# Performance work log

Measured on AMD Instinct MI355X. Metric: run time of the kernel, lower is better.

## Reference

```python
import jax, jax.numpy as jnp
import numpy as np

N_NODES = 50000
N_EDGES = 1_600_000
IN_CH = 128
OUT_CH = 64
HEADS = 2
NEG_SLOPE = 0.2  # PyG GATConv default negative_slope


def setup_inputs() -> dict:
    key = jax.random.key(0)
    ks = jax.random.split(key, 8)
    x = jax.random.normal(ks[0], (N_NODES, IN_CH), dtype=jnp.float32)
    edge_index = jax.random.randint(ks[1], (2, N_EDGES), 0, N_NODES, dtype=jnp.int64)
    edge_weight = jax.random.uniform(ks[2], (N_EDGES,), dtype=jnp.float32)
    W = jax.random.normal(ks[3], (IN_CH, HEADS * OUT_CH), dtype=jnp.float32) * (1.0 / np.sqrt(IN_CH))
    att_src = jax.random.normal(ks[4], (HEADS, OUT_CH), dtype=jnp.float32) * (1.0 / np.sqrt(OUT_CH))
    att_dst = jax.random.normal(ks[5], (HEADS, OUT_CH), dtype=jnp.float32) * (1.0 / np.sqrt(OUT_CH))
    bias = jnp.zeros((HEADS * OUT_CH,), dtype=jnp.float32)
    return {"x": x, "edge_index": edge_index, "edge_weight": edge_weight,
            "W": W, "att_src": att_src, "att_dst": att_dst, "bias": bias}


def reference(x, edge_index, edge_weight, W, att_src, att_dst, bias):
    # GATLayer: zero-masking is a no-op multiply (x * (x != 0)), kept for faithfulness.
    x_masked = x * (x != 0.0).astype(x.dtype)

    # GATConv (concat=True, add_self_loops=True). edge_weight is passed as edge_attr
    # but edge_dim is None, so it does not enter the attention math (legacy PyG behavior).
    n = x.shape[0]
    xp = (x_masked @ W).reshape(n, HEADS, OUT_CH)  # [N, H, C]

    # add self loops
    loops = jnp.arange(n, dtype=edge_index.dtype)
    src = jnp.concatenate([edge_index[0], loops])
    dst = jnp.concatenate([edge_index[1], loops])

    a_src = jnp.einsum('nhc,hc->nh', xp, att_src)  # [N, H]
    a_dst = jnp.einsum('nhc,hc->nh', xp, att_dst)  # [N, H]

    alpha = jax.nn.leaky_relu(a_src[src] + a_dst[dst], NEG_SLOPE)  # [E', H]

    # per-destination segment softmax
    m = jax.ops.segment_max(alpha, dst, num_segments=n)
    e = jnp.exp(alpha - m[dst])
    s = jax.ops.segment_sum(e, dst, num_segments=n)
    alpha = e / (s[dst] + 1e-16)

    # dropout on attention coefficients skipped (eval mode / deterministic baseline)
    msg = alpha[:, :, None] * xp[src]  # [E', H, C]
    out = jax.ops.segment_sum(msg, dst, num_segments=n)  # [N, H, C]
    return out.reshape(n, HEADS * OUT_CH) + bias
```

## Files before the change

### kernel.cpp

```cpp
#include <hip/hip_runtime.h>
#include <hip/hip_bf16.h>

#define NN 50000
#define NE 1600000
#define NE2 (NE + NN)
#define NEG_SLOPE 0.2f
#define NBUCK 196
#define BCAP 10240
#define P1E 4096
#define P1B ((NE2 + P1E - 1) / P1E)

__device__ __forceinline__ float bflo(unsigned u) { return __uint_as_float(u << 16); }
__device__ __forceinline__ float bfhi(unsigned u) { return __uint_as_float(u & 0xffff0000u); }
__device__ __forceinline__ float rlanef(float v, int l) {
    return __uint_as_float(__builtin_amdgcn_readlane(__float_as_uint(v), l));
}

__global__ __launch_bounds__(256, 4) void k_gemm(const float* __restrict__ x,
                                                 const float* __restrict__ W,
                                                 const float* __restrict__ att_src,
                                                 const float* __restrict__ att_dst,
                                                 __hip_bfloat16* __restrict__ xpb,
                                                 float* __restrict__ a4) {
    __shared__ float xl[64][128];
    const int tid = threadIdx.x;
    const int n0 = blockIdx.x * 64;
    const int rows_here = min(64, NN - n0);
    {
        const float4* xg = (const float4*)(x + (size_t)n0 * 128);
        float4* xl4 = (float4*)&xl[0][0];
        const int cnt = rows_here * 32;
        for (int i = tid; i < cnt; i += 256) xl4[i] = xg[i];
    }
    __syncthreads();

    const int c = tid & 127;
    const int half = tid >> 7;
    const int h = c >> 6;
    const int cc = c & 63;
    const float at_s = att_src[h * 64 + cc];
    const float at_d = att_dst[h * 64 + cc];

    float acc[32];
    #pragma unroll
    for (int r = 0; r < 32; r++) acc[r] = 0.f;

    #pragma unroll 2
    for (int kq = 0; kq < 32; kq++) {
        const float w0 = W[(kq * 4 + 0) * 128 + c];
        const float w1 = W[(kq * 4 + 1) * 128 + c];
        const float w2 = W[(kq * 4 + 2) * 128 + c];
        const float w3 = W[(kq * 4 + 3) * 128 + c];
        #pragma unroll
        for (int r = 0; r < 32; r++) {
            const float4 xv = *(const float4*)&xl[half * 32 + r][kq * 4];
            acc[r] = fmaf(xv.x, w0, acc[r]);
            acc[r] = fmaf(xv.y, w1, acc[r]);
            acc[r] = fmaf(xv.z, w2, acc[r]);
            acc[r] = fmaf(xv.w, w3, acc[r]);
        }
    }

    const int lane = tid & 63;
    #pragma unroll 4
    for (int r = 0; r < 32; r++) {
        const int n = n0 + half * 32 + r;
        if (n < NN) {
            xpb[(size_t)n * 128 + c] = __float2bfloat16(acc[r]);
            float vs = acc[r] * at_s;
            float vd = acc[r] * at_d;
            #pragma unroll
            for (int o = 32; o > 0; o >>= 1) {
                vs += __shfl_xor(vs, o);
                vd += __shfl_xor(vd, o);
            }
            if (lane == 0) {
                a4[(size_t)n * 4 + h]     = vs;
                a4[(size_t)n * 4 + 2 + h] = vd;
            }
        }
    }
}

__global__ __launch_bounds__(256) void k_part(const int* __restrict__ ei,
                                              int* __restrict__ gcur,
                                              unsigned int* __restrict__ grecs) {
    __shared__ unsigned int rec[P1E];
    __shared__ unsigned short bk[P1E];
    __shared__ int h[NBUCK], bas[NBUCK], cur[NBUCK];
    const int t = threadIdx.x;
    const int e0 = blockIdx.x * P1E;
    const int n = min(P1E, NE2 - e0);
    for (int i = t; i < NBUCK; i += 256) h[i] = 0;
    __syncthreads();
    for (int i = t; i < n; i += 256) {
        const int e = e0 + i;
        int src, dst;
        if (e < NE) { src = ei[e]; dst = ei[NE + e]; }
        else        { src = dst = e - NE; }
        const int b = dst >> 8;
        rec[i] = ((unsigned)(dst & 255) << 16) | (unsigned)src;
        bk[i] = (unsigned short)b;
        atomicAdd(&h[b], 1);
    }
    __syncthreads();
    for (int i = t; i < NBUCK; i += 256) {
        bas[i] = (h[i] > 0) ? atomicAdd(&gcur[i], h[i]) : 0;
        cur[i] = 0;
    }
    __syncthreads();
    for (int i = t; i < n; i += 256) {
        const int b = bk[i];
        const int p = bas[b] + atomicAdd(&cur[b], 1);
        if (p < BCAP) grecs[(size_t)b * BCAP + p] = rec[i];
    }
}

__global__ __launch_bounds__(256) void k_bscan(const int* __restrict__ gcur,
                                               int* __restrict__ cbase) {
    __shared__ int s[256];
    const int t = threadIdx.x;
    const int v = (t < NBUCK) ? gcur[t] : 0;
    s[t] = v;
    __syncthreads();
    for (int o = 1; o < 256; o <<= 1) {
        const int u = (t >= o) ? s[t - o] : 0;
        __syncthreads();
        s[t] += u;
        __syncthreads();
    }
    if (t < NBUCK) cbase[t] = s[t] - v;
}

__global__ __launch_bounds__(256) void k_sortb(const unsigned int* __restrict__ grecs,
                                               const int* __restrict__ gcur,
                                               const int* __restrict__ cbase,
                                               unsigned short* __restrict__ csr,
                                               int* __restrict__ off) {
    __shared__ int h[256], o[256], c[256], s[256];
    const int b = blockIdx.x;
    const int t = threadIdx.x;
    const int nb = min(gcur[b], BCAP);
    const int base = cbase[b];
    const unsigned int* r = grecs + (size_t)b * BCAP;
    h[t] = 0;
    __syncthreads();
    for (int i = t; i < nb; i += 256) atomicAdd(&h[r[i] >> 16], 1);
    __syncthreads();
    const int v = h[t];
    s[t] = v;
    __syncthreads();
    for (int k = 1; k < 256; k <<= 1) {
        const int u = (t >= k) ? s[t - k] : 0;
        __syncthreads();
        s[t] += u;
        __syncthreads();
    }
    o[t] = s[t] - v;
    c[t] = 0;
    const int d = b * 256 + t;
    if (d < NN) off[d] = base + o[t];
    if (b == 0 && t == 0) off[NN] = NE2;
    __syncthreads();
    for (int i = t; i < nb; i += 256) {
        const unsigned int rr = r[i];
        const int dl = rr >> 16;
        const int slot = atomicAdd(&c[dl], 1);
        csr[base + o[dl] + slot] = (unsigned short)(rr & 0xffffu);
    }
}

__global__ __launch_bounds__(256) void k_accum(const unsigned short* __restrict__ csr,
                                               const int* __restrict__ off,
                                               const float* __restrict__ a4,
                                               const unsigned short* __restrict__ xpb,
                                               const float* __restrict__ bias,
                                               float* __restrict__ out) {
    const int lane = threadIdx.x & 63;
    const int d = blockIdx.x * 4 + (threadIdx.x >> 6);
    if (d >= NN) return;
    const int o0 = off[d];
    const int ne = off[d + 1] - o0;
    const float4 ad4 = ((const float4*)a4)[d];
    const int q = lane & 31;
    const int hsel = q >> 4;
    const bool isA = lane < 32;

    float acc0 = 0.f, acc1 = 0.f, acc2 = 0.f, acc3 = 0.f;
    float s0 = 0.f, s1 = 0.f;

    for (int base = 0; base < ne; base += 64) {
        const int cnt = min(ne - base, 64);
        int src = 0;
        float e0 = 0.f, e1 = 0.f;
        if (lane < cnt) {
            src = csr[o0 + base + lane];
            const float4 as4 = ((const float4*)a4)[src];
            float l0 = as4.x + ad4.z;
            float l1 = as4.y + ad4.w;
            l0 = (l0 > 0.f) ? l0 : NEG_SLOPE * l0;
            l1 = (l1 > 0.f) ? l1 : NEG_SLOPE * l1;
            e0 = __expf(l0);
            e1 = __expf(l1);
        }
        s0 += e0;
        s1 += e1;
        for (int j = 0; j < cnt; j += 2) {
            const int   sA  = __builtin_amdgcn_readlane(src, j);
            const int   sB  = __builtin_amdgcn_readlane(src, j + 1);
            const float wA0 = rlanef(e0, j);
            const float wA1 = rlanef(e1, j);
            const float wB0 = rlanef(e0, j + 1);
            const float wB1 = rlanef(e1, j + 1);
            const int   s   = isA ? sA : sB;
            const float w   = isA ? (hsel ? wA1 : wA0) : (hsel ? wB1 : wB0);
            const uint2 pv = *(const uint2*)(xpb + (size_t)s * 128 + q * 4);
            acc0 = fmaf(w, bflo(pv.x), acc0);
            acc1 = fmaf(w, bfhi(pv.x), acc1);
            acc2 = fmaf(w, bflo(pv.y), acc2);
            acc3 = fmaf(w, bfhi(pv.y), acc3);
        }
    }
    #pragma unroll
    for (int o = 32; o > 0; o >>= 1) {
        s0 += __shfl_xor(s0, o);
        s1 += __shfl_xor(s1, o);
    }
    acc0 += __shfl_xor(acc0, 32);
    acc1 += __shfl_xor(acc1, 32);
    acc2 += __shfl_xor(acc2, 32);
    acc3 += __shfl_xor(acc3, 32);
    if (isA) {
        const float inv = 1.0f / ((hsel ? s1 : s0) + 1e-16f);
        const float4 bv = ((const float4*)bias)[q];
        float4 ov;
        ov.x = acc0 * inv + bv.x;
        ov.y = acc1 * inv + bv.y;
        ov.z = acc2 * inv + bv.z;
        ov.w = acc3 * inv + bv.w;
        ((float4*)(out + (size_t)d * 128))[q] = ov;
    }
}

extern "C" void kernel_launch(void* const* d_in, const int* in_sizes, int n_in,
                              void* d_out, int out_size, void* d_ws, size_t ws_size,
                              hipStream_t stream) {
    const float* x    = (const float*)d_in[0];
    const int*   ei   = (const int*)d_in[1];
    const float* W    = (const float*)d_in[3];
    const float* atts = (const float*)d_in[4];
    const float* attd = (const float*)d_in[5];
    const float* bias = (const float*)d_in[6];
    float* out = (float*)d_out;

    char* ws = (char*)d_ws;
    __hip_bfloat16* xpb = (__hip_bfloat16*)ws;
    float* a4      = (float*)(ws + 12800000);
    int*   gcur    = (int*)  (ws + 13600000);
    int*   cbase   = (int*)  (ws + 13601024);
    int*   off     = (int*)  (ws + 13602048);
    unsigned short* csr = (unsigned short*)(ws + 13802112);
    unsigned int* grecs = (unsigned int*)(ws + 17102112);

    hipMemsetAsync(gcur, 0, NBUCK * sizeof(int), stream);
    k_gemm <<<(NN + 63) / 64, 256, 0, stream>>>(x, W, atts, attd, xpb, a4);
    k_part <<<P1B, 256, 0, stream>>>(ei, gcur, grecs);
    k_bscan<<<1, 256, 0, stream>>>(gcur, cbase);
    k_sortb<<<NBUCK, 256, 0, stream>>>(grecs, gcur, cbase, csr, off);
    k_accum<<<(NN + 3) / 4, 256, 0, stream>>>(csr, off, a4, (const unsigned short*)xpb, bias, out);
}
```

Measured before the change: 265.7 us.

## Retile projection GEMM into 4x4 register micro-tiles with 32-row blocks

Rewrites the x@W projection kernel so each thread computes a 4-row by 4-column register tile, using float4 loads of W and shared x, instead of one column across 32 rows. Block rows drop from 64 to 32, which halves shared memory and doubles the grid, and the occupancy hint goes from 4 to 6. The attention dot products now reduce over 16 lanes with shuffles and bf16 outputs are stored as packed 8-byte writes. The intent is fewer scalar W loads, fewer accumulator registers and higher occupancy. The cost is more global reads of W per output row.

Result: faster. 239.9 us (-9.7%).

```diff
diff --git a/kernel.cpp b/kernel.cpp
--- a/kernel.cpp
+++ b/kernel.cpp
@@ -16,16 +16,16 @@
     return __uint_as_float(__builtin_amdgcn_readlane(__float_as_uint(v), l));
 }
 
-__global__ __launch_bounds__(256, 4) void k_gemm(const float* __restrict__ x,
+__global__ __launch_bounds__(256, 6) void k_gemm(const float* __restrict__ x,
                                                  const float* __restrict__ W,
                                                  const float* __restrict__ att_src,
                                                  const float* __restrict__ att_dst,
                                                  __hip_bfloat16* __restrict__ xpb,
                                                  float* __restrict__ a4) {
-    __shared__ float xl[64][128];
+    __shared__ float xl[32][128];
     const int tid = threadIdx.x;
-    const int n0 = blockIdx.x * 64;
-    const int rows_here = min(64, NN - n0);
+    const int n0 = blockIdx.x * 32;
+    const int rows_here = min(32, NN - n0);
     {
         const float4* xg = (const float4*)(x + (size_t)n0 * 128);
         float4* xl4 = (float4*)&xl[0][0];
@@ -34,50 +34,75 @@
     }
     __syncthreads();
 
-    const int c = tid & 127;
-    const int half = tid >> 7;
-    const int h = c >> 6;
-    const int cc = c & 63;
-    const float at_s = att_src[h * 64 + cc];
-    const float at_d = att_dst[h * 64 + cc];
-
-    float acc[32];
+    const int cq = tid & 31;
+    const int c0 = cq * 4;
+    const int rg = tid >> 5;
+    const int r0 = rg * 4;
+
+    float acc[4][4];
     #pragma unroll
-    for (int r = 0; r < 32; r++) acc[r] = 0.f;
-
-    #pragma unroll 2
-    for (int kq = 0; kq < 32; kq++) {
-        const float w0 = W[(kq * 4 + 0) * 128 + c];
-        const float w1 = W[(kq * 4 + 1) * 128 + c];
-        const float w2 = W[(kq * 4 + 2) * 128 + c];
-        const float w3 = W[(kq * 4 + 3) * 128 + c];
-        #pragma unroll
-        for (int r = 0; r < 32; r++) {
-            const float4 xv = *(const float4*)&xl[half * 32 + r][kq * 4];
-            acc[r] = fmaf(xv.x, w0, acc[r]);
-            acc[r] = fmaf(xv.y, w1, acc[r]);
-            acc[r] = fmaf(xv.z, w2, acc[r]);
-            acc[r] = fmaf(xv.w, w3, acc[r]);
-        }
-    }
-
-    const int lane = tid & 63;
+    for (int r = 0; r < 4; r++)
+        #pragma unroll
+        for (int c = 0; c < 4; c++) acc[r][c] = 0.f;
+
     #pragma unroll 4
-    for (int r = 0; r < 32; r++) {
-        const int n = n0 + half * 32 + r;
-        if (n < NN) {
-            xpb[(size_t)n * 128 + c] = __float2bfloat16(acc[r]);
-            float vs = acc[r] * at_s;
-            float vd = acc[r] * at_d;
-            #pragma unroll
-            for (int o = 32; o > 0; o >>= 1) {
-                vs += __shfl_xor(vs, o);
-                vd += __shfl_xor(vd, o);
-            }
-            if (lane == 0) {
-                a4[(size_t)n * 4 + h]     = vs;
-                a4[(size_t)n * 4 + 2 + h] = vd;
-            }
+    for (int k = 0; k < 128; k += 4) {
+        float4 wv[4];
+        #pragma unroll
+        for (int kk = 0; kk < 4; kk++)
+            wv[kk] = *(const float4*)&W[(size_t)(k + kk) * 128 + c0];
+        float4 xv[4];
+        #pragma unroll
+        for (int r = 0; r < 4; r++)
+            xv[r] = *(const float4*)&xl[r0 + r][k];
+        #pragma unroll
+        for (int r = 0; r < 4; r++) {
+            acc[r][0] = fmaf(xv[r].x, wv[0].x, acc[r][0]);
+            acc[r][1] = fmaf(xv[r].x, wv[0].y, acc[r][1]);
+            acc[r][2] = fmaf(xv[r].x, wv[0].z, acc[r][2]);
+            acc[r][3] = fmaf(xv[r].x, wv[0].w, acc[r][3]);
+            acc[r][0] = fmaf(xv[r].y, wv[1].x, acc[r][0]);
+            acc[r][1] = fmaf(xv[r].y, wv[1].y, acc[r][1]);
+            acc[r][2] = fmaf(xv[r].y, wv[1].z, acc[r][2]);
+            acc[r][3] = fmaf(xv[r].y, wv[1].w, acc[r][3]);
+            acc[r][0] = fmaf(xv[r].z, wv[2].x, acc[r][0]);
+            acc[r][1] = fmaf(xv[r].z, wv[2].y, acc[r][1]);
+            acc[r][2] = fmaf(xv[r].z, wv[2].z, acc[r][2]);
+            acc[r][3] = fmaf(xv[r].z, wv[2].w, acc[r][3]);
+            acc[r][0] = fmaf(xv[r].w, wv[3].x, acc[r][0]);
+            acc[r][1] = fmaf(xv[r].w, wv[3].y, acc[r][1]);
+            acc[r][2] = fmaf(xv[r].w, wv[3].z, acc[r][2]);
+            acc[r][3] = fmaf(xv[r].w, wv[3].w, acc[r][3]);
+        }
+    }
+
+    const float4 ats = *(const float4*)&att_src[c0];
+    const float4 atd = *(const float4*)&att_dst[c0];
+    #pragma unroll
+    for (int r = 0; r < 4; r++) {
+        const int n = n0 + r0 + r;
+        const bool ok = (n < NN);
+        if (ok) {
+            __hip_bfloat16 hb[4];
+            hb[0] = __float2bfloat16(acc[r][0]);
+            hb[1] = __float2bfloat16(acc[r][1]);
+            hb[2] = __float2bfloat16(acc[r][2]);
+            hb[3] = __float2bfloat16(acc[r][3]);
+            *(uint2*)&xpb[(size_t)n * 128 + c0] = *(uint2*)hb;
+        }
+        float vs = acc[r][0] * ats.x + acc[r][1] * ats.y +
+                   acc[r][2] * ats.z + acc[r][3] * ats.w;
+        float vd = acc[r][0] * atd.x + acc[r][1] * atd.y +
+                   acc[r][2] * atd.z + acc[r][3] * atd.w;
+        #pragma unroll
+        for (int m = 8; m > 0; m >>= 1) {
+            vs += __shfl_xor(vs, m);
+            vd += __shfl_xor(vd, m);
+        }
+        if (ok && (cq & 15) == 0) {
+            const int h = cq >> 4;
+            a4[(size_t)n * 4 + h]     = vs;
+            a4[(size_t)n * 4 + 2 + h] = vd;
         }
     }
 }
@@ -263,7 +288,7 @@
     unsigned int* grecs = (unsigned int*)(ws + 17102112);
 
     hipMemsetAsync(gcur, 0, NBUCK * sizeof(int), stream);
-    k_gemm <<<(NN + 63) / 64, 256, 0, stream>>>(x, W, atts, attd, xpb, a4);
+    k_gemm <<<(NN + 31) / 32, 256, 0, stream>>>(x, W, atts, attd, xpb, a4);
     k_part <<<P1B, 256, 0, stream>>>(ei, gcur, grecs);
     k_bscan<<<1, 256, 0, stream>>>(gcur, cbase);
     k_sortb<<<NBUCK, 256, 0, stream>>>(grecs, gcur, cbase, csr, off);
```
